# Kernel optimization log

Hardware: AMD Instinct MI355X
Metric: run time of the kernel (lower is better)

The kernel has to match this reference:

```python
import jax, jax.numpy as jnp
import numpy as np

MODEL_DIM = 512
NUM_HEADS = 8
HEAD_DIM = MODEL_DIM // NUM_HEADS  # 64
NUM_NODE = 1024
CLUSTER = 128
S = 60
EMBED = 0.5


def setup_inputs() -> dict:
    key = jax.random.key(0)
    ks = jax.random.split(key, 16)
    d = MODEL_DIM
    sc = 1.0 / np.sqrt(d)
    inp = {
        "x": jax.random.normal(ks[0], (4, 12, NUM_NODE, d), dtype=jnp.float32),
        "Wq": jax.random.normal(ks[1], (d, d), dtype=jnp.float32) * sc,
        "bq": jnp.zeros((d,), jnp.float32),
        "Wk": jax.random.normal(ks[2], (d, d), dtype=jnp.float32) * sc,
        "bk": jnp.zeros((d,), jnp.float32),
        "Wv": jax.random.normal(ks[3], (d, d), dtype=jnp.float32) * sc,
        "bv": jnp.zeros((d,), jnp.float32),
        "We": jax.random.normal(ks[4], (d, d), dtype=jnp.float32) * sc,
        "be": jnp.zeros((d,), jnp.float32),
        "Wo": jax.random.normal(ks[5], (d, d), dtype=jnp.float32) * sc,
        "bo": jnp.zeros((d,), jnp.float32),
        # adp_pos is initialized to zeros in torch; use small randn for a non-degenerate test
        "adp_pos": jax.random.normal(ks[6], (NUM_NODE, CLUSTER), dtype=jnp.float32) * 0.02,
        "U1": jax.random.normal(ks[7], (HEAD_DIM, S), dtype=jnp.float32) * np.sqrt(2.0 / (HEAD_DIM + S)),
        "U2": jax.random.normal(ks[8], (S, HEAD_DIM), dtype=jnp.float32) * np.sqrt(2.0 / (S + HEAD_DIM)),
    }
    return inp


def _split_heads(t):
    # torch.cat(torch.split(t, head_dim, -1), 0): heads stacked head-major on batch dim
    return jnp.concatenate(jnp.split(t, NUM_HEADS, axis=-1), axis=0)


def _merge_heads(t):
    return jnp.concatenate(jnp.split(t, NUM_HEADS, axis=0), axis=-1)


def _pool_nodes(t):
    # AdaptiveAvgPool2d((CLUSTER, None)) on (B,T,N,D) with N % CLUSTER == 0 -> block mean
    B, T, N, D = t.shape
    return t.reshape(B, T, CLUSTER, N // CLUSTER, D).mean(axis=3)


def reference(x, Wq, bq, Wk, bk, Wv, bv, We, be, Wo, bo, adp_pos, U1, U2):
    q = x @ Wq.T + bq                      # (B,T,N,D)
    k = _pool_nodes(x @ Wk.T + bk)          # (B,T,C,D)
    v = _pool_nodes(x @ Wv.T + bv)          # (B,T,C,D)
    ev = x @ We.T + be                      # (B,T,N,D)

    qh = _split_heads(q)                    # (B*H,T,N,d)
    kh = _split_heads(k)                    # (B*H,T,C,d)
    vh = _split_heads(v)                    # (B*H,T,C,d)
    evh = _split_heads(ev)                  # (B*H,T,N,d)

    # external attention branch: softmax over node dim (-2)
    exa = jax.nn.softmax(evh @ U1, axis=-2)  # (B*H,T,N,S)
    exa_val = (exa @ U2) * EMBED + evh       # (B*H,T,N,d)

    score = jnp.einsum("btnd,btcd->btnc", qh, kh) / np.sqrt(HEAD_DIM)
    score = score + adp_pos[None, None]      # (B*H,T,N,C)
    attn = jax.nn.softmax(score, axis=-1)

    out = attn @ vh + exa_val                # (B*H,T,N,d)
    out = _merge_heads(out)                  # (B,T,N,D)
    return out @ Wo.T + bo
```

## Files before the change

kernel.cpp:

```cpp
#include <hip/hip_runtime.h>


#define LOG2E 1.44269504088896f

typedef __attribute__((ext_vector_type(4))) float f32x4;
typedef __attribute__((ext_vector_type(8))) short bf16x8;

__device__ __forceinline__ unsigned short f2bf(float f) {
    union { float f; unsigned u; } v; v.f = f;
    unsigned r = (v.u + 0x7fffu + ((v.u >> 16) & 1u)) >> 16;
    return (unsigned short)r;
}
__device__ __forceinline__ float bf2f(unsigned short h) {
    union { unsigned u; float f; } v; v.u = ((unsigned)h) << 16;
    return v.f;
}
__device__ __forceinline__ unsigned cvt_pk_bf16(float lo, float hi) {
    unsigned r;
    asm("v_cvt_pk_bf16_f32 %0, %1, %2" : "=v"(r) : "v"(lo), "v"(hi));
    return r;
}
__device__ __forceinline__ void gll16(const void* g, void* l) {
    __builtin_amdgcn_global_load_lds((const __attribute__((address_space(1))) void*)g,
                                     (__attribute__((address_space(3))) void*)l,
                                     16, 0, 0);
}

__global__ void cvt_w(const float* __restrict__ Wq, const float* __restrict__ Wk,
                      const float* __restrict__ Wv, const float* __restrict__ We,
                      const float* __restrict__ Wo, const float* __restrict__ U1,
                      const float* __restrict__ U2,
                      const float* __restrict__ bq, const float* __restrict__ bk,
                      const float* __restrict__ bv, const float* __restrict__ be,
                      unsigned short* __restrict__ Wqe, unsigned short* __restrict__ Wkv,
                      unsigned short* __restrict__ Wob, unsigned short* __restrict__ U1T,
                      unsigned short* __restrict__ U2bT,
                      float* __restrict__ bqe, float* __restrict__ bkv)
{
    int i = blockIdx.x * 256 + threadIdx.x;
    if (i < 524288) {
        int r = i >> 9;
        float v = (r < 512) ? Wq[i] * 0.125f : We[i - 262144];
        Wqe[i] = f2bf(v);
    } else if (i < 1048576) {
        int j = i - 524288; int r = j >> 9;
        float v = (r < 512) ? Wk[j] : Wv[j - 262144];
        Wkv[j] = f2bf(v);
    } else if (i < 1310720) {
        int j = i - 1048576;
        Wob[j] = f2bf(Wo[j]);
    } else if (i < 1314816) {
        int j = i - 1310720; int s = j >> 6, k = j & 63;
        U1T[j] = (s < 60) ? f2bf(U1[k * 60 + s]) : (unsigned short)0;
    } else if (i < 1318912) {
        int j = i - 1314816; int d = j >> 6, s = j & 63;
        U2bT[j] = (s < 60) ? f2bf(U2[s * 64 + d] * 0.5f) : (unsigned short)0;
    } else if (i < 1319936) {
        int j = i - 1318912;
        bqe[j] = (j < 512) ? bq[j] * 0.125f : be[j - 512];
    } else if (i < 1320960) {
        int j = i - 1319936;
        bkv[j] = (j < 512) ? bk[j] : bv[j - 512];
    }
}

__global__ void cvt_pool(const float* __restrict__ x, unsigned short* __restrict__ xb,
                         unsigned short* __restrict__ xpb)
{
    int i = blockIdx.x * 256 + threadIdx.x;
    int d4 = i & 127;
    int btc = i >> 7;
    int bt = btc >> 7, c = btc & 127;
    long base = ((long)(bt * 1024 + c * 8)) * 128 + d4;
    const float4* src = (const float4*)x + base;
    ushort4* dst = (ushort4*)xb + base;
    float sx = 0.f, sy = 0.f, sz = 0.f, sw = 0.f;
#pragma unroll
    for (int j = 0; j < 8; j++) {
        float4 v = src[(long)j * 128];
        sx += v.x; sy += v.y; sz += v.z; sw += v.w;
        ushort4 o;
        o.x = f2bf(v.x); o.y = f2bf(v.y); o.z = f2bf(v.z); o.w = f2bf(v.w);
        dst[(long)j * 128] = o;
    }
    ushort4 p;
    p.x = f2bf(sx * 0.125f); p.y = f2bf(sy * 0.125f);
    p.z = f2bf(sz * 0.125f); p.w = f2bf(sw * 0.125f);
    ((ushort4*)xpb)[(long)btc * 128 + d4] = p;
}

__global__ __launch_bounds__(256, 4) void g1_qev(
    const unsigned short* __restrict__ A, const unsigned short* __restrict__ W,
    const float* __restrict__ bias, unsigned short* __restrict__ qh,
    unsigned short* __restrict__ evh)
{
    const int K = 512;
    __shared__ __attribute__((aligned(16))) unsigned short As[128 * 32];
    __shared__ __attribute__((aligned(16))) unsigned short Bs[128 * 32];
    const int tid = threadIdx.x;
    const int wave = tid >> 6, lane = tid & 63;
    const int quad = lane >> 4, l16 = lane & 15;
    const int b = blockIdx.x, xcd = b & 7, j = b >> 3;
    const int m0 = (((j >> 3) << 3) + xcd) * 128, n0 = (j & 7) * 128;
    const int wm = (wave & 1) * 64, wn = (wave >> 1) * 64;

    f32x4 acc[4][4];
#pragma unroll
    for (int i = 0; i < 4; i++)
#pragma unroll
        for (int jj = 0; jj < 4; jj++) acc[i][jj] = (f32x4){0.f, 0.f, 0.f, 0.f};

    const int c0 = tid, c1 = tid + 256;
    const int r0 = c0 >> 2, kc0 = (c0 & 3) * 8;
    const int r1 = c1 >> 2, kc1 = (c1 & 3) * 8;
    const unsigned short* pa0 = A + (long)(m0 + r0) * K + kc0;
    const unsigned short* pa1 = A + (long)(m0 + r1) * K + kc1;
    const unsigned short* pb0 = W + (long)(n0 + r0) * K + kc0;
    const unsigned short* pb1 = W + (long)(n0 + r1) * K + kc1;
    unsigned short* lA0 = &As[wave * 512];
    unsigned short* lA1 = &As[2048 + wave * 512];
    unsigned short* lB0 = &Bs[wave * 512];
    unsigned short* lB1 = &Bs[2048 + wave * 512];

    for (int k0 = 0; k0 < K; k0 += 32) {
        gll16(pa0 + k0, lA0);
        gll16(pa1 + k0, lA1);
        gll16(pb0 + k0, lB0);
        gll16(pb1 + k0, lB1);
        __syncthreads();
        bf16x8 af[4], bfr[4];
#pragma unroll
        for (int t = 0; t < 4; t++)
            af[t] = *(const bf16x8*)&As[(wm + t * 16 + l16) * 32 + quad * 8];
#pragma unroll
        for (int t = 0; t < 4; t++)
            bfr[t] = *(const bf16x8*)&Bs[(wn + t * 16 + l16) * 32 + quad * 8];
#pragma unroll
        for (int tm = 0; tm < 4; tm++)
#pragma unroll
            for (int tn = 0; tn < 4; tn++)
                acc[tm][tn] = __builtin_amdgcn_mfma_f32_16x16x32_bf16(
                    af[tm], bfr[tn], acc[tm][tn], 0, 0, 0);
        __syncthreads();
    }

#pragma unroll
    for (int tm = 0; tm < 4; tm++)
#pragma unroll
        for (int tn = 0; tn < 4; tn++) {
            int cc = n0 + wn + tn * 16 + l16;
            float bv = bias[cc];
            int hq = (cc >> 6) & 7, dd = cc & 63;
            int rr0 = m0 + wm + tm * 16 + quad * 4;
            int bt = rr0 >> 10, n = rr0 & 1023;
            unsigned short* dst = ((cc < 512) ? qh : evh)
                + ((long)(bt * 8 + hq) * 1024 + n) * 64 + dd;
#pragma unroll
            for (int r = 0; r < 4; r++)
                dst[(long)r * 64] = f2bf(acc[tm][tn][r] + bv);
        }
}

template <int NTL2>
__global__ __launch_bounds__(256, 4) void gemm_bt(
    const unsigned short* __restrict__ A, const unsigned short* __restrict__ W,
    const float* __restrict__ bias, float* __restrict__ Cout,
    int N, int K)
{
    __shared__ __attribute__((aligned(16))) unsigned short As[128 * 32];
    __shared__ __attribute__((aligned(16))) unsigned short Bs[128 * 32];
    const int tid = threadIdx.x;
    const int wave = tid >> 6, lane = tid & 63;
    const int quad = lane >> 4, l16 = lane & 15;
    const int b = blockIdx.x, xcd = b & 7, j = b >> 3;
    const int m0 = (((j >> NTL2) << 3) + xcd) * 128;
    const int n0 = (j & ((1 << NTL2) - 1)) * 128;
    const int wm = (wave & 1) * 64, wn = (wave >> 1) * 64;

    f32x4 acc[4][4];
#pragma unroll
    for (int i = 0; i < 4; i++)
#pragma unroll
        for (int jj = 0; jj < 4; jj++) acc[i][jj] = (f32x4){0.f, 0.f, 0.f, 0.f};

    const int c0 = tid, c1 = tid + 256;
    const int r0 = c0 >> 2, kc0 = (c0 & 3) * 8;
    const int r1 = c1 >> 2, kc1 = (c1 & 3) * 8;
    const unsigned short* pa0 = A + (long)(m0 + r0) * K + kc0;
    const unsigned short* pa1 = A + (long)(m0 + r1) * K + kc1;
    const unsigned short* pb0 = W + (long)(n0 + r0) * K + kc0;
    const unsigned short* pb1 = W + (long)(n0 + r1) * K + kc1;
    unsigned short* lA0 = &As[wave * 512];
    unsigned short* lA1 = &As[2048 + wave * 512];
    unsigned short* lB0 = &Bs[wave * 512];
    unsigned short* lB1 = &Bs[2048 + wave * 512];

    for (int k0 = 0; k0 < K; k0 += 32) {
        gll16(pa0 + k0, lA0);
        gll16(pa1 + k0, lA1);
        gll16(pb0 + k0, lB0);
        gll16(pb1 + k0, lB1);
        __syncthreads();
        bf16x8 af[4], bfr[4];
#pragma unroll
        for (int t = 0; t < 4; t++)
            af[t] = *(const bf16x8*)&As[(wm + t * 16 + l16) * 32 + quad * 8];
#pragma unroll
        for (int t = 0; t < 4; t++)
            bfr[t] = *(const bf16x8*)&Bs[(wn + t * 16 + l16) * 32 + quad * 8];
#pragma unroll
        for (int tm = 0; tm < 4; tm++)
#pragma unroll
            for (int tn = 0; tn < 4; tn++)
                acc[tm][tn] = __builtin_amdgcn_mfma_f32_16x16x32_bf16(
                    af[tm], bfr[tn], acc[tm][tn], 0, 0, 0);
        __syncthreads();
    }

#pragma unroll
    for (int tm = 0; tm < 4; tm++)
#pragma unroll
        for (int tn = 0; tn < 4; tn++) {
            int cc = n0 + wn + tn * 16 + l16;
            float bv = bias[cc];
#pragma unroll
            for (int r = 0; r < 4; r++) {
                int rr = m0 + wm + tm * 16 + quad * 4 + r;
                Cout[(long)rr * N + cc] = acc[tm][tn][r] + bv;
            }
        }
}

__global__ __launch_bounds__(256, 4) void g2_kv(
    const unsigned short* __restrict__ A, const unsigned short* __restrict__ W,
    const float* __restrict__ bias, unsigned short* __restrict__ kvK,
    unsigned short* __restrict__ vT)
{
    const int K = 512;
    __shared__ __attribute__((aligned(16))) unsigned short As[128 * 32];
    __shared__ __attribute__((aligned(16))) unsigned short Bs[128 * 32];
    const int tid = threadIdx.x;
    const int wave = tid >> 6, lane = tid & 63;
    const int quad = lane >> 4, l16 = lane & 15;
    const int b = blockIdx.x, xcd = b & 7, j = b >> 3;
    const int m0 = (((j >> 3) << 3) + xcd) * 128, n0 = (j & 7) * 128;
    const int wm = (wave & 1) * 64, wn = (wave >> 1) * 64;

    f32x4 acc[4][4];
#pragma unroll
    for (int i = 0; i < 4; i++)
#pragma unroll
        for (int jj = 0; jj < 4; jj++) acc[i][jj] = (f32x4){0.f, 0.f, 0.f, 0.f};

    const int c0 = tid, c1 = tid + 256;
    const int r0 = c0 >> 2, kc0 = (c0 & 3) * 8;
    const int r1 = c1 >> 2, kc1 = (c1 & 3) * 8;
    const unsigned short* pa0 = A + (long)(m0 + r0) * K + kc0;
    const unsigned short* pa1 = A + (long)(m0 + r1) * K + kc1;
    const unsigned short* pb0 = W + (long)(n0 + r0) * K + kc0;
    const unsigned short* pb1 = W + (long)(n0 + r1) * K + kc1;
    unsigned short* lA0 = &As[wave * 512];
    unsigned short* lA1 = &As[2048 + wave * 512];
    unsigned short* lB0 = &Bs[wave * 512];
    unsigned short* lB1 = &Bs[2048 + wave * 512];

    for (int k0 = 0; k0 < K; k0 += 32) {
        gll16(pa0 + k0, lA0);
        gll16(pa1 + k0, lA1);
        gll16(pb0 + k0, lB0);
        gll16(pb1 + k0, lB1);
        __syncthreads();
        bf16x8 af[4], bfr[4];
#pragma unroll
        for (int t = 0; t < 4; t++)
            af[t] = *(const bf16x8*)&As[(wm + t * 16 + l16) * 32 + quad * 8];
#pragma unroll
        for (int t = 0; t < 4; t++)
            bfr[t] = *(const bf16x8*)&Bs[(wn + t * 16 + l16) * 32 + quad * 8];
#pragma unroll
        for (int tm = 0; tm < 4; tm++)
#pragma unroll
            for (int tn = 0; tn < 4; tn++)
                acc[tm][tn] = __builtin_amdgcn_mfma_f32_16x16x32_bf16(
                    af[tm], bfr[tn], acc[tm][tn], 0, 0, 0);
        __syncthreads();
    }

#pragma unroll
    for (int tm = 0; tm < 4; tm++)
#pragma unroll
        for (int tn = 0; tn < 4; tn++) {
            int cc = n0 + wn + tn * 16 + l16;
            float bv = bias[cc];
            int rrb = m0 + wm + tm * 16 + quad * 4;
            if (cc < 512) {
#pragma unroll
                for (int r = 0; r < 4; r++)
                    kvK[(long)(rrb + r) * 512 + cc] = f2bf(acc[tm][tn][r] + bv);
            } else {
                int hh = (cc - 512) >> 6, dd = (cc - 512) & 63;
                int btv = rrb >> 7, cv = rrb & 127;
                ushort4 o;
                o.x = f2bf(acc[tm][tn][0] + bv);
                o.y = f2bf(acc[tm][tn][1] + bv);
                o.z = f2bf(acc[tm][tn][2] + bv);
                o.w = f2bf(acc[tm][tn][3] + bv);
                *(ushort4*)(vT + ((long)(btv * 8 + hh) * 64 + dd) * 128 + cv) = o;
            }
        }
}

__global__ __launch_bounds__(256, 4) void ez_kernel(
    const unsigned short* __restrict__ evh, const unsigned short* __restrict__ U1T,
    unsigned short* __restrict__ Z, float* __restrict__ pM, float* __restrict__ pL)
{
    __shared__ __attribute__((aligned(16))) unsigned short evs[128 * 72];
    __shared__ __attribute__((aligned(16))) unsigned short u1s[64 * 72];
    __shared__ float ms4[4][64];
    __shared__ float ls4[4][64];
    int tid = threadIdx.x, bx = blockIdx.x;
    int bt = bx >> 6, h = (bx >> 3) & 7, nb = bx & 7;
    int wave = tid >> 6, lane = tid & 63, quad = lane >> 4, l16 = lane & 15;
    long gb = ((long)(bt * 8 + h) * 1024 + nb * 128) * 64;

#pragma unroll
    for (int i = 0; i < 4; i++) {
        int c = tid + i * 256; int row = c >> 3, kc = (c & 7) * 8;
        *(int4*)&evs[row * 72 + kc] = *(const int4*)(evh + gb + row * 64 + kc);
    }
#pragma unroll
    for (int i = 0; i < 2; i++) {
        int c = tid + i * 256; int row = c >> 3, kc = (c & 7) * 8;
        *(int4*)&u1s[row * 72 + kc] = *(const int4*)(U1T + row * 64 + kc);
    }
    __syncthreads();

    f32x4 acc[2][4];
#pragma unroll
    for (int i = 0; i < 2; i++)
#pragma unroll
        for (int t = 0; t < 4; t++) acc[i][t] = (f32x4){0.f, 0.f, 0.f, 0.f};

#pragma unroll
    for (int kt = 0; kt < 2; kt++) {
        bf16x8 a[2], b[4];
#pragma unroll
        for (int i = 0; i < 2; i++)
            a[i] = *(const bf16x8*)&evs[((wave * 2 + i) * 16 + l16) * 72 + kt * 32 + quad * 8];
#pragma unroll
        for (int t = 0; t < 4; t++)
            b[t] = *(const bf16x8*)&u1s[(t * 16 + l16) * 72 + kt * 32 + quad * 8];
#pragma unroll
        for (int i = 0; i < 2; i++)
#pragma unroll
            for (int t = 0; t < 4; t++)
                acc[i][t] = __builtin_amdgcn_mfma_f32_16x16x32_bf16(a[i], b[t], acc[i][t], 0, 0, 0);
    }

    long zb = (long)(bt * 8 + h) * 1024 + nb * 128;
    unsigned short zr[2][4][4];
#pragma unroll
    for (int i = 0; i < 2; i++)
#pragma unroll
        for (int t = 0; t < 4; t++) {
            int s = t * 16 + l16;
#pragma unroll
            for (int r = 0; r < 4; r++) zr[i][t][r] = f2bf(acc[i][t][r]);
            if (s < 60) {
#pragma unroll
                for (int r = 0; r < 4; r++) {
                    int rr = (wave * 2 + i) * 16 + quad * 4 + r;
                    Z[(zb + rr) * 60 + s] = zr[i][t][r];
                }
            }
        }

    float mp[4], lp[4];
#pragma unroll
    for (int t = 0; t < 4; t++) {
        float m = -1e30f;
#pragma unroll
        for (int i = 0; i < 2; i++)
#pragma unroll
            for (int r = 0; r < 4; r++) m = fmaxf(m, bf2f(zr[i][t][r]));
        float l = 0.f;
#pragma unroll
        for (int i = 0; i < 2; i++)
#pragma unroll
            for (int r = 0; r < 4; r++) l += exp2f((bf2f(zr[i][t][r]) - m) * LOG2E);
        mp[t] = m; lp[t] = l;
    }
#pragma unroll
    for (int d = 16; d <= 32; d <<= 1)
#pragma unroll
        for (int t = 0; t < 4; t++) {
            float mo = __shfl_xor(mp[t], d, 64);
            float lo = __shfl_xor(lp[t], d, 64);
            float nm = fmaxf(mp[t], mo);
            lp[t] = lp[t] * exp2f((mp[t] - nm) * LOG2E) + lo * exp2f((mo - nm) * LOG2E);
            mp[t] = nm;
        }
    if (quad == 0) {
#pragma unroll
        for (int t = 0; t < 4; t++) {
            ms4[wave][t * 16 + l16] = mp[t];
            ls4[wave][t * 16 + l16] = lp[t];
        }
    }
    __syncthreads();
    if (tid < 64) {
        float M = ms4[0][tid];
#pragma unroll
        for (int w = 1; w < 4; w++) M = fmaxf(M, ms4[w][tid]);
        float L = 0.f;
#pragma unroll
        for (int w = 0; w < 4; w++) L += ls4[w][tid] * exp2f((ms4[w][tid] - M) * LOG2E);
        pM[(long)bx * 64 + tid] = M;
        pL[(long)bx * 64 + tid] = L;
    }
}

__global__ void es_reduce(const float* __restrict__ pM, const float* __restrict__ pL,
                          float* __restrict__ mS, float* __restrict__ lSinv)
{
    int g = blockIdx.x, s = threadIdx.x;
    float mv[8], lv[8], M = -1e30f;
#pragma unroll
    for (int nb = 0; nb < 8; nb++) {
        mv[nb] = pM[(long)(g * 8 + nb) * 64 + s];
        lv[nb] = pL[(long)(g * 8 + nb) * 64 + s];
        M = fmaxf(M, mv[nb]);
    }
    float L = 0.f;
#pragma unroll
    for (int nb = 0; nb < 8; nb++) L += lv[nb] * exp2f((mv[nb] - M) * LOG2E);
    if (s < 60) {
        mS[g * 60 + s] = M;
        lSinv[g * 60 + s] = 1.0f / L;
    }
}

__global__ __launch_bounds__(256, 4) void att_kernel(
    const unsigned short* __restrict__ qh, const unsigned short* __restrict__ evh,
    const unsigned short* __restrict__ kvK, const unsigned short* __restrict__ vT,
    const unsigned short* __restrict__ Z,
    const float* __restrict__ mS, const float* __restrict__ lI,
    const float* __restrict__ adp, const unsigned short* __restrict__ U2bT,
    unsigned short* __restrict__ attn_out)
{
    __shared__ __attribute__((aligned(16))) unsigned short Ps[128 * 136];

    int tid = threadIdx.x, bx = blockIdx.x;
    int bt = bx >> 6, h = (bx >> 3) & 7, nb = bx & 7;
    int wave = tid >> 6, lane = tid & 63, quad = lane >> 4, l16 = lane & 15;
    int n0 = nb * 128;
    const int g = bt * 8 + h;
    const long grow0 = (long)g * 1024 + n0;

    f32x4 sc[2][8];
#pragma unroll
    for (int i = 0; i < 2; i++)
#pragma unroll
        for (int t = 0; t < 8; t++) sc[i][t] = (f32x4){0.f, 0.f, 0.f, 0.f};

#pragma unroll
    for (int kt = 0; kt < 2; kt++) {
        bf16x8 qf[2];
#pragma unroll
        for (int i = 0; i < 2; i++)
            qf[i] = *(const bf16x8*)(qh + (grow0 + wave * 32 + i * 16 + l16) * 64
                                     + kt * 32 + quad * 8);
#pragma unroll
        for (int tn = 0; tn < 8; tn++) {
            bf16x8 kf = *(const bf16x8*)(kvK + (long)(bt * 128 + tn * 16 + l16) * 512
                                         + h * 64 + kt * 32 + quad * 8);
#pragma unroll
            for (int i = 0; i < 2; i++)
                sc[i][tn] = __builtin_amdgcn_mfma_f32_16x16x32_bf16(kf, qf[i], sc[i][tn], 0, 0, 0);
        }
    }

#pragma unroll
    for (int i = 0; i < 2; i++) {
        const int qr = wave * 32 + i * 16 + l16;
        float m = -1e30f;
#pragma unroll
        for (int tn = 0; tn < 8; tn++) {
            float4 ad = *(const float4*)(adp + (long)(n0 + qr) * 128 + tn * 16 + quad * 4);
            sc[i][tn][0] += ad.x; sc[i][tn][1] += ad.y;
            sc[i][tn][2] += ad.z; sc[i][tn][3] += ad.w;
#pragma unroll
            for (int r = 0; r < 4; r++) m = fmaxf(m, sc[i][tn][r]);
        }
        m = fmaxf(m, __shfl_xor(m, 16, 64));
        m = fmaxf(m, __shfl_xor(m, 32, 64));
        float s = 0.f;
#pragma unroll
        for (int tn = 0; tn < 8; tn++)
#pragma unroll
            for (int r = 0; r < 4; r++) {
                float p = exp2f((sc[i][tn][r] - m) * LOG2E);
                sc[i][tn][r] = p; s += p;
            }
        s += __shfl_xor(s, 16, 64);
        s += __shfl_xor(s, 32, 64);
        float rinv = 1.0f / s;
#pragma unroll
        for (int tn = 0; tn < 8; tn++) {
            uint2 w2;
            w2.x = cvt_pk_bf16(sc[i][tn][0] * rinv, sc[i][tn][1] * rinv);
            w2.y = cvt_pk_bf16(sc[i][tn][2] * rinv, sc[i][tn][3] * rinv);
            *(uint2*)&Ps[qr * 136 + tn * 16 + quad * 4] = w2;
        }
    }

    f32x4 oc[2][4];
#pragma unroll
    for (int i = 0; i < 2; i++)
#pragma unroll
        for (int t = 0; t < 4; t++) oc[i][t] = (f32x4){0.f, 0.f, 0.f, 0.f};

#pragma unroll
    for (int kt = 0; kt < 4; kt++) {
        bf16x8 a[2];
#pragma unroll
        for (int i = 0; i < 2; i++)
            a[i] = *(const bf16x8*)&Ps[(wave * 32 + i * 16 + l16) * 136 + kt * 32 + quad * 8];
        __builtin_amdgcn_s_setprio(1);
#pragma unroll
        for (int tn = 0; tn < 4; tn++) {
            bf16x8 b = *(const bf16x8*)(vT + ((long)g * 64 + tn * 16 + l16) * 128
                                        + kt * 32 + quad * 8);
#pragma unroll
            for (int i = 0; i < 2; i++)
                oc[i][tn] = __builtin_amdgcn_mfma_f32_16x16x32_bf16(a[i], b, oc[i][tn], 0, 0, 0);
        }
        __builtin_amdgcn_s_setprio(0);
    }

#pragma unroll
    for (int kt = 0; kt < 2; kt++) {
        int sb = kt * 32 + quad * 8;
        float4 ma = *(const float4*)(mS + (long)g * 60 + sb);
        float4 mb2 = *(const float4*)(mS + (long)g * 60 + sb + 4);
        float4 la = *(const float4*)(lI + (long)g * 60 + sb);
        float4 lb2 = *(const float4*)(lI + (long)g * 60 + sb + 4);
        float mv[8] = {ma.x, ma.y, ma.z, ma.w, mb2.x, mb2.y, mb2.z, mb2.w};
        float lv[8] = {la.x, la.y, la.z, la.w, lb2.x, lb2.y, lb2.z, lb2.w};
        bf16x8 ea[2];
#pragma unroll
        for (int i = 0; i < 2; i++) {
            int row = wave * 32 + i * 16 + l16;
            const unsigned short* zp = Z + ((long)g * 1024 + n0 + row) * 60 + sb;
            uint2 z0 = *(const uint2*)zp;
            uint2 z1 = *(const uint2*)(zp + 4);
            unsigned zz[4] = {z0.x, z0.y, z1.x, z1.y};
            unsigned short es_[8];
#pragma unroll
            for (int jj = 0; jj < 8; jj++) {
                unsigned short zh = (unsigned short)((zz[jj >> 1] >> ((jj & 1) * 16)) & 0xffff);
                float e = (sb + jj < 60)
                    ? exp2f((bf2f(zh) - mv[jj]) * LOG2E) * lv[jj] : 0.f;
                es_[jj] = f2bf(e);
            }
            ea[i] = *(bf16x8*)es_;
        }
        __builtin_amdgcn_s_setprio(1);
#pragma unroll
        for (int tn = 0; tn < 4; tn++) {
            bf16x8 b = *(const bf16x8*)(U2bT + (tn * 16 + l16) * 64 + sb);
#pragma unroll
            for (int i = 0; i < 2; i++)
                oc[i][tn] = __builtin_amdgcn_mfma_f32_16x16x32_bf16(ea[i], b, oc[i][tn], 0, 0, 0);
        }
        __builtin_amdgcn_s_setprio(0);
    }

#pragma unroll
    for (int i = 0; i < 2; i++)
#pragma unroll
        for (int tn = 0; tn < 4; tn++)
#pragma unroll
            for (int r = 0; r < 4; r++) {
                int rr = wave * 32 + i * 16 + quad * 4 + r;
                int cc = tn * 16 + l16;
                float ev = bf2f(evh[(grow0 + rr) * 64 + cc]);
                attn_out[((long)bt * 1024 + n0 + rr) * 512 + h * 64 + cc]
                    = f2bf(oc[i][tn][r] + ev);
            }
}

extern "C" void kernel_launch(void* const* d_in, const int* in_sizes, int n_in,
                              void* d_out, int out_size, void* d_ws, size_t ws_size,
                              hipStream_t stream)
{
    const float* x   = (const float*)d_in[0];
    const float* Wq  = (const float*)d_in[1];
    const float* bq  = (const float*)d_in[2];
    const float* Wk  = (const float*)d_in[3];
    const float* bk  = (const float*)d_in[4];
    const float* Wv  = (const float*)d_in[5];
    const float* bv  = (const float*)d_in[6];
    const float* We  = (const float*)d_in[7];
    const float* be  = (const float*)d_in[8];
    const float* Wo  = (const float*)d_in[9];
    const float* bo  = (const float*)d_in[10];
    const float* adp = (const float*)d_in[11];
    const float* U1  = (const float*)d_in[12];
    const float* U2  = (const float*)d_in[13];

    char* ws = (char*)d_ws;
    unsigned short* xb   = (unsigned short*)(ws + 0);
    unsigned short* aout = xb;
    float*          pMb  = (float*)(ws + 0);
    float*          pLb  = (float*)(ws + 786432);
    unsigned short* xpb  = (unsigned short*)(ws + 50331648);
    unsigned short* qh   = (unsigned short*)(ws + 56623104);
    unsigned short* evh  = (unsigned short*)(ws + 106954752);
    unsigned short* kvK  = (unsigned short*)(ws + 157286400);
    unsigned short* vT   = (unsigned short*)(ws + 163577856);
    unsigned short* Zb   = (unsigned short*)(ws + 169869312);
    unsigned short* Wqe  = (unsigned short*)(ws + 217055232);
    unsigned short* Wkv  = (unsigned short*)(ws + 218103808);
    unsigned short* Wob  = (unsigned short*)(ws + 219152384);
    unsigned short* U1T  = (unsigned short*)(ws + 219676672);
    unsigned short* U2bT = (unsigned short*)(ws + 219684864);
    float*          mSb  = (float*)(ws + 219693056);
    float*          lIb  = (float*)(ws + 219785216);
    float*          bqe  = (float*)(ws + 219877376);
    float*          bkv  = (float*)(ws + 219881472);

    cvt_w<<<5160, 256, 0, stream>>>(Wq, Wk, Wv, We, Wo, U1, U2, bq, bk, bv, be,
                                    Wqe, Wkv, Wob, U1T, U2bT, bqe, bkv);
    cvt_pool<<<3072, 256, 0, stream>>>(x, xb, xpb);

    g1_qev<<<3072, 256, 0, stream>>>(xb, Wqe, bqe, qh, evh);
    g2_kv<<<384, 256, 0, stream>>>(xpb, Wkv, bkv, kvK, vT);

    ez_kernel<<<3072, 256, 0, stream>>>(evh, U1T, Zb, pMb, pLb);
    es_reduce<<<384, 64, 0, stream>>>(pMb, pLb, mSb, lIb);
    att_kernel<<<3072, 256, 0, stream>>>(qh, evh, kvK, vT, Zb, mSb, lIb, adp, U2bT, aout);

    gemm_bt<2><<<1536, 256, 0, stream>>>(aout, Wob, bo, (float*)d_out, 512, 512);
}
```

Baseline: 436.8 us.

## Recompute external-attention logits in att_kernel instead of storing Z

The ez_kernel no longer writes the bf16 logit tensor Z to global memory. It only computes per-block softmax max and sum statistics, reading evh and U1T directly without staging them in LDS. att_kernel recomputes the evh·U1 logits with MFMA, applies exp2 against a single log-sum-exp offset produced by es_reduce, writes the probabilities into the Ps shared buffer and multiplies by U2. LOG2E is folded into U1T so the exp2 calls skip a multiply. This removes a roughly 47MB write and read round trip in exchange for duplicated MFMA work and extra register pressure in att_kernel.

After: 446.1 us. 2.1% more time.

```diff
diff --git a/kernel.cpp b/kernel.cpp
--- a/kernel.cpp
+++ b/kernel.cpp
@@ -51,7 +51,7 @@
         Wob[j] = f2bf(Wo[j]);
     } else if (i < 1314816) {
         int j = i - 1310720; int s = j >> 6, k = j & 63;
-        U1T[j] = (s < 60) ? f2bf(U1[k * 60 + s]) : (unsigned short)0;
+        U1T[j] = (s < 60) ? f2bf(U1[k * 60 + s] * LOG2E) : (unsigned short)0;
     } else if (i < 1318912) {
         int j = i - 1314816; int d = j >> 6, s = j & 63;
         U2bT[j] = (s < 60) ? f2bf(U2[s * 64 + d] * 0.5f) : (unsigned short)0;
@@ -312,28 +312,14 @@
 
 __global__ __launch_bounds__(256, 4) void ez_kernel(
     const unsigned short* __restrict__ evh, const unsigned short* __restrict__ U1T,
-    unsigned short* __restrict__ Z, float* __restrict__ pM, float* __restrict__ pL)
-{
-    __shared__ __attribute__((aligned(16))) unsigned short evs[128 * 72];
-    __shared__ __attribute__((aligned(16))) unsigned short u1s[64 * 72];
+    float* __restrict__ pM, float* __restrict__ pL)
+{
     __shared__ float ms4[4][64];
     __shared__ float ls4[4][64];
     int tid = threadIdx.x, bx = blockIdx.x;
     int bt = bx >> 6, h = (bx >> 3) & 7, nb = bx & 7;
     int wave = tid >> 6, lane = tid & 63, quad = lane >> 4, l16 = lane & 15;
-    long gb = ((long)(bt * 8 + h) * 1024 + nb * 128) * 64;
-
-#pragma unroll
-    for (int i = 0; i < 4; i++) {
-        int c = tid + i * 256; int row = c >> 3, kc = (c & 7) * 8;
-        *(int4*)&evs[row * 72 + kc] = *(const int4*)(evh + gb + row * 64 + kc);
-    }
-#pragma unroll
-    for (int i = 0; i < 2; i++) {
-        int c = tid + i * 256; int row = c >> 3, kc = (c & 7) * 8;
-        *(int4*)&u1s[row * 72 + kc] = *(const int4*)(U1T + row * 64 + kc);
-    }
-    __syncthreads();
+    long gb0 = (long)(bt * 8 + h) * 1024 + nb * 128;
 
     f32x4 acc[2][4];
 #pragma unroll
@@ -346,10 +332,11 @@
         bf16x8 a[2], b[4];
 #pragma unroll
         for (int i = 0; i < 2; i++)
-            a[i] = *(const bf16x8*)&evs[((wave * 2 + i) * 16 + l16) * 72 + kt * 32 + quad * 8];
-#pragma unroll
-        for (int t = 0; t < 4; t++)
-            b[t] = *(const bf16x8*)&u1s[(t * 16 + l16) * 72 + kt * 32 + quad * 8];
+            a[i] = *(const bf16x8*)(evh + (gb0 + (wave * 2 + i) * 16 + l16) * 64
+                                    + kt * 32 + quad * 8);
+#pragma unroll
+        for (int t = 0; t < 4; t++)
+            b[t] = *(const bf16x8*)(U1T + (t * 16 + l16) * 64 + kt * 32 + quad * 8);
 #pragma unroll
         for (int i = 0; i < 2; i++)
 #pragma unroll
@@ -357,24 +344,6 @@
                 acc[i][t] = __builtin_amdgcn_mfma_f32_16x16x32_bf16(a[i], b[t], acc[i][t], 0, 0, 0);
     }
 
-    long zb = (long)(bt * 8 + h) * 1024 + nb * 128;
-    unsigned short zr[2][4][4];
-#pragma unroll
-    for (int i = 0; i < 2; i++)
-#pragma unroll
-        for (int t = 0; t < 4; t++) {
-            int s = t * 16 + l16;
-#pragma unroll
-            for (int r = 0; r < 4; r++) zr[i][t][r] = f2bf(acc[i][t][r]);
-            if (s < 60) {
-#pragma unroll
-                for (int r = 0; r < 4; r++) {
-                    int rr = (wave * 2 + i) * 16 + quad * 4 + r;
-                    Z[(zb + rr) * 60 + s] = zr[i][t][r];
-                }
-            }
-        }
-
     float mp[4], lp[4];
 #pragma unroll
     for (int t = 0; t < 4; t++) {
@@ -382,12 +351,12 @@
 #pragma unroll
         for (int i = 0; i < 2; i++)
 #pragma unroll
-            for (int r = 0; r < 4; r++) m = fmaxf(m, bf2f(zr[i][t][r]));
+            for (int r = 0; r < 4; r++) m = fmaxf(m, acc[i][t][r]);
         float l = 0.f;
 #pragma unroll
         for (int i = 0; i < 2; i++)
 #pragma unroll
-            for (int r = 0; r < 4; r++) l += exp2f((bf2f(zr[i][t][r]) - m) * LOG2E);
+            for (int r = 0; r < 4; r++) l += exp2f(acc[i][t][r] - m);
         mp[t] = m; lp[t] = l;
     }
 #pragma unroll
@@ -397,7 +366,7 @@
             float mo = __shfl_xor(mp[t], d, 64);
             float lo = __shfl_xor(lp[t], d, 64);
             float nm = fmaxf(mp[t], mo);
-            lp[t] = lp[t] * exp2f((mp[t] - nm) * LOG2E) + lo * exp2f((mo - nm) * LOG2E);
+            lp[t] = lp[t] * exp2f(mp[t] - nm) + lo * exp2f(mo - nm);
             mp[t] = nm;
         }
     if (quad == 0) {
@@ -414,14 +383,14 @@
         for (int w = 1; w < 4; w++) M = fmaxf(M, ms4[w][tid]);
         float L = 0.f;
 #pragma unroll
-        for (int w = 0; w < 4; w++) L += ls4[w][tid] * exp2f((ms4[w][tid] - M) * LOG2E);
+        for (int w = 0; w < 4; w++) L += ls4[w][tid] * exp2f(ms4[w][tid] - M);
         pM[(long)bx * 64 + tid] = M;
         pL[(long)bx * 64 + tid] = L;
     }
 }
 
 __global__ void es_reduce(const float* __restrict__ pM, const float* __restrict__ pL,
-                          float* __restrict__ mS, float* __restrict__ lSinv)
+                          float* __restrict__ dS)
 {
     int g = blockIdx.x, s = threadIdx.x;
     float mv[8], lv[8], M = -1e30f;
@@ -433,19 +402,15 @@
     }
     float L = 0.f;
 #pragma unroll
-    for (int nb = 0; nb < 8; nb++) L += lv[nb] * exp2f((mv[nb] - M) * LOG2E);
-    if (s < 60) {
-        mS[g * 60 + s] = M;
-        lSinv[g * 60 + s] = 1.0f / L;
-    }
+    for (int nb = 0; nb < 8; nb++) L += lv[nb] * exp2f(mv[nb] - M);
+    dS[(long)g * 64 + s] = (s < 60) ? (M + __log2f(L)) : 1e30f;
 }
 
 __global__ __launch_bounds__(256, 4) void att_kernel(
     const unsigned short* __restrict__ qh, const unsigned short* __restrict__ evh,
     const unsigned short* __restrict__ kvK, const unsigned short* __restrict__ vT,
-    const unsigned short* __restrict__ Z,
-    const float* __restrict__ mS, const float* __restrict__ lI,
-    const float* __restrict__ adp, const unsigned short* __restrict__ U2bT,
+    const float* __restrict__ dS, const float* __restrict__ adp,
+    const unsigned short* __restrict__ U1T, const unsigned short* __restrict__ U2bT,
     unsigned short* __restrict__ attn_out)
 {
     __shared__ __attribute__((aligned(16))) unsigned short Ps[128 * 136];
@@ -514,6 +479,32 @@
         }
     }
 
+    f32x4 za[2][4];
+#pragma unroll
+    for (int i = 0; i < 2; i++)
+#pragma unroll
+        for (int t = 0; t < 4; t++) za[i][t] = (f32x4){0.f, 0.f, 0.f, 0.f};
+#pragma unroll
+    for (int kt = 0; kt < 2; kt++) {
+        bf16x8 u1f[4], evf[2];
+#pragma unroll
+        for (int t = 0; t < 4; t++)
+            u1f[t] = *(const bf16x8*)(U1T + (t * 16 + l16) * 64 + kt * 32 + quad * 8);
+#pragma unroll
+        for (int i = 0; i < 2; i++)
+            evf[i] = *(const bf16x8*)(evh + (grow0 + wave * 32 + i * 16 + l16) * 64
+                                      + kt * 32 + quad * 8);
+#pragma unroll
+        for (int i = 0; i < 2; i++)
+#pragma unroll
+            for (int t = 0; t < 4; t++)
+                za[i][t] = __builtin_amdgcn_mfma_f32_16x16x32_bf16(u1f[t], evf[i], za[i][t], 0, 0, 0);
+    }
+    float4 dv[4];
+#pragma unroll
+    for (int t = 0; t < 4; t++)
+        dv[t] = *(const float4*)(dS + (long)g * 64 + t * 16 + quad * 4);
+
     f32x4 oc[2][4];
 #pragma unroll
     for (int i = 0; i < 2; i++)
@@ -526,7 +517,6 @@
 #pragma unroll
         for (int i = 0; i < 2; i++)
             a[i] = *(const bf16x8*)&Ps[(wave * 32 + i * 16 + l16) * 136 + kt * 32 + quad * 8];
-        __builtin_amdgcn_s_setprio(1);
 #pragma unroll
         for (int tn = 0; tn < 4; tn++) {
             bf16x8 b = *(const bf16x8*)(vT + ((long)g * 64 + tn * 16 + l16) * 128
@@ -535,45 +525,37 @@
             for (int i = 0; i < 2; i++)
                 oc[i][tn] = __builtin_amdgcn_mfma_f32_16x16x32_bf16(a[i], b, oc[i][tn], 0, 0, 0);
         }
-        __builtin_amdgcn_s_setprio(0);
+    }
+
+#pragma unroll
+    for (int i = 0; i < 2; i++) {
+        const int row = wave * 32 + i * 16 + l16;
+#pragma unroll
+        for (int t = 0; t < 4; t++) {
+            float e0 = exp2f(za[i][t][0] - dv[t].x);
+            float e1 = exp2f(za[i][t][1] - dv[t].y);
+            float e2 = exp2f(za[i][t][2] - dv[t].z);
+            float e3 = exp2f(za[i][t][3] - dv[t].w);
+            uint2 w2;
+            w2.x = cvt_pk_bf16(e0, e1);
+            w2.y = cvt_pk_bf16(e2, e3);
+            *(uint2*)&Ps[row * 136 + t * 16 + quad * 4] = w2;
+        }
     }
 
 #pragma unroll
     for (int kt = 0; kt < 2; kt++) {
-        int sb = kt * 32 + quad * 8;
-        float4 ma = *(const float4*)(mS + (long)g * 60 + sb);
-        float4 mb2 = *(const float4*)(mS + (long)g * 60 + sb + 4);
-        float4 la = *(const float4*)(lI + (long)g * 60 + sb);
-        float4 lb2 = *(const float4*)(lI + (long)g * 60 + sb + 4);
-        float mv[8] = {ma.x, ma.y, ma.z, ma.w, mb2.x, mb2.y, mb2.z, mb2.w};
-        float lv[8] = {la.x, la.y, la.z, la.w, lb2.x, lb2.y, lb2.z, lb2.w};
-        bf16x8 ea[2];
-#pragma unroll
-        for (int i = 0; i < 2; i++) {
-            int row = wave * 32 + i * 16 + l16;
-            const unsigned short* zp = Z + ((long)g * 1024 + n0 + row) * 60 + sb;
-            uint2 z0 = *(const uint2*)zp;
-            uint2 z1 = *(const uint2*)(zp + 4);
-            unsigned zz[4] = {z0.x, z0.y, z1.x, z1.y};
-            unsigned short es_[8];
-#pragma unroll
-            for (int jj = 0; jj < 8; jj++) {
-                unsigned short zh = (unsigned short)((zz[jj >> 1] >> ((jj & 1) * 16)) & 0xffff);
-                float e = (sb + jj < 60)
-                    ? exp2f((bf2f(zh) - mv[jj]) * LOG2E) * lv[jj] : 0.f;
-                es_[jj] = f2bf(e);
-            }
-            ea[i] = *(bf16x8*)es_;
-        }
-        __builtin_amdgcn_s_setprio(1);
+        bf16x8 eaf[2];
+#pragma unroll
+        for (int i = 0; i < 2; i++)
+            eaf[i] = *(const bf16x8*)&Ps[(wave * 32 + i * 16 + l16) * 136 + kt * 32 + quad * 8];
 #pragma unroll
         for (int tn = 0; tn < 4; tn++) {
-            bf16x8 b = *(const bf16x8*)(U2bT + (tn * 16 + l16) * 64 + sb);
+            bf16x8 b = *(const bf16x8*)(U2bT + (tn * 16 + l16) * 64 + kt * 32 + quad * 8);
 #pragma unroll
             for (int i = 0; i < 2; i++)
-                oc[i][tn] = __builtin_amdgcn_mfma_f32_16x16x32_bf16(ea[i], b, oc[i][tn], 0, 0, 0);
-        }
-        __builtin_amdgcn_s_setprio(0);
+                oc[i][tn] = __builtin_amdgcn_mfma_f32_16x16x32_bf16(eaf[i], b, oc[i][tn], 0, 0, 0);
+        }
     }
 
 #pragma unroll
@@ -619,14 +601,12 @@
     unsigned short* evh  = (unsigned short*)(ws + 106954752);
     unsigned short* kvK  = (unsigned short*)(ws + 157286400);
     unsigned short* vT   = (unsigned short*)(ws + 163577856);
-    unsigned short* Zb   = (unsigned short*)(ws + 169869312);
+    float*          dSb  = (float*)(ws + 169869312);
     unsigned short* Wqe  = (unsigned short*)(ws + 217055232);
     unsigned short* Wkv  = (unsigned short*)(ws + 218103808);
     unsigned short* Wob  = (unsigned short*)(ws + 219152384);
     unsigned short* U1T  = (unsigned short*)(ws + 219676672);
     unsigned short* U2bT = (unsigned short*)(ws + 219684864);
-    float*          mSb  = (float*)(ws + 219693056);
-    float*          lIb  = (float*)(ws + 219785216);
     float*          bqe  = (float*)(ws + 219877376);
     float*          bkv  = (float*)(ws + 219881472);
 
@@ -637,9 +617,9 @@
     g1_qev<<<3072, 256, 0, stream>>>(xb, Wqe, bqe, qh, evh);
     g2_kv<<<384, 256, 0, stream>>>(xpb, Wkv, bkv, kvK, vT);
 
-    ez_kernel<<<3072, 256, 0, stream>>>(evh, U1T, Zb, pMb, pLb);
-    es_reduce<<<384, 64, 0, stream>>>(pMb, pLb, mSb, lIb);
-    att_kernel<<<3072, 256, 0, stream>>>(qh, evh, kvK, vT, Zb, mSb, lIb, adp, U2bT, aout);
+    ez_kernel<<<3072, 256, 0, stream>>>(evh, U1T, pMb, pLb);
+    es_reduce<<<384, 64, 0, stream>>>(pMb, pLb, dSb);
+    att_kernel<<<3072, 256, 0, stream>>>(qh, evh, kvK, vT, dSb, adp, U1T, U2bT, aout);
 
     gemm_bt<2><<<1536, 256, 0, stream>>>(aout, Wob, bo, (float*)d_out, 512, 512);
 }
```
